# Kernel optimization log

Measured on AMD Instinct MI355X. Metric: run time of the kernel, lower is better.

The kernel has to match this reference:

```python
import jax, jax.numpy as jnp
import numpy as np

B, T, C, H = 8, 2048, 1024, 128


def setup_inputs() -> dict:
    key = jax.random.key(0)
    k1, k2, k3, k4 = jax.random.split(key, 4)
    x = jax.random.normal(k1, (B, T, C), dtype=jnp.float32)
    # torch nn.Linear(n_embed, head_size, bias=False) weights, stored as [C, H] for x @ W
    scale = 1.0 / np.sqrt(C)
    Wk = jax.random.normal(k2, (C, H), dtype=jnp.float32) * scale
    Wq = jax.random.normal(k3, (C, H), dtype=jnp.float32) * scale
    Wv = jax.random.normal(k4, (C, H), dtype=jnp.float32) * scale
    return {"x": x, "Wk": Wk, "Wq": Wq, "Wv": Wv}


def reference(x, Wk, Wq, Wv):
    # Faithful translation of Head.forward (dropout = identity in eval mode).
    Bx, Tx, Cx = x.shape
    k = x @ Wk  # [B,T,H]
    q = x @ Wq  # [B,T,H]
    v = x @ Wv  # [B,T,H]
    # NOTE: original scales by C**-0.5 (n_embed), not head_size**-0.5.
    scores = jnp.einsum('bth,bsh->bts', q, k) * (Cx ** -0.5)  # [B,T,T]
    causal = jnp.tril(jnp.ones((Tx, Tx), dtype=bool))  # tril buffer
    scores = jnp.where(causal, scores, -jnp.inf)
    weights = jax.nn.softmax(scores, axis=-1)
    out = jnp.einsum('bts,bsh->bth', weights, v)  # [B,T,H]
    return out
```

## Files before the change

### kernel.cpp

```cpp
#include <hip/hip_runtime.h>
#include <type_traits>

#define Bn 8
#define Tn 2048
#define Cn 1024
#define Hn 128
#define Mn (Bn*Tn)

typedef __attribute__((ext_vector_type(4))) float f32x4;
typedef __attribute__((ext_vector_type(2))) float f32x2;
typedef __attribute__((ext_vector_type(16))) float f32x16;
typedef __attribute__((ext_vector_type(8))) short s16x8;
typedef __attribute__((ext_vector_type(4))) int i32x4;
typedef __attribute__((ext_vector_type(2))) int i32x2;
typedef unsigned int u32;

__device__ __forceinline__ unsigned short f2bf(float f) {
  union { float f; unsigned u; } v; v.f = f;
  unsigned r = v.u + 0x7FFFu + ((v.u >> 16) & 1u);
  return (unsigned short)(r >> 16);
}

__device__ __forceinline__ unsigned cvtpk(float lo, float hi) {
  unsigned r;
  asm("v_cvt_pk_bf16_f32 %0, %1, %2" : "=v"(r) : "v"(lo), "v"(hi));
  return r;
}

__device__ __forceinline__ i32x2 swap32(int a, int b) {
#if __has_builtin(__builtin_amdgcn_permlane32_swap)
  return __builtin_amdgcn_permlane32_swap(a, b, false, false);
#else
  int ax = __shfl_xor(a, 32), bx = __shfl_xor(b, 32);
  i32x2 r;
  r[0] = (threadIdx.x & 32) ? bx : a;
  r[1] = (threadIdx.x & 32) ? b : ax;
  return r;
#endif
}

__device__ __forceinline__ void gl_lds16(const void* g, void* l) {
  __builtin_amdgcn_global_load_lds((const __attribute__((address_space(1))) u32*)g,
                                   (__attribute__((address_space(3))) u32*)l, 16, 0, 0);
}

__global__ __launch_bounds__(256) void prep_wt(const float* __restrict__ Wq,
                                               const float* __restrict__ Wk,
                                               const float* __restrict__ Wv,
                                               unsigned short* __restrict__ Wt) {
  __shared__ float tile[64][33];
  const int w = blockIdx.z;
  const float* W = (w == 0) ? Wq : (w == 1) ? Wk : Wv;
  const float scale = (w == 0) ? 0.03125f : 1.0f;
  const int c0 = blockIdx.x * 64, h0 = blockIdx.y * 32;
  const int tid = threadIdx.x;
  const int hl = tid & 31, cg = tid >> 5;
#pragma unroll
  for (int i = 0; i < 8; i++) {
    int cl = cg * 8 + i;
    tile[cl][hl] = W[(c0 + cl) * Hn + h0 + hl];
  }
  __syncthreads();
  const int cl2 = tid & 63, hg = tid >> 6;
#pragma unroll
  for (int i = 0; i < 8; i++) {
    int hl2 = hg * 8 + i;
    Wt[(size_t)(w * Hn + h0 + hl2) * Cn + c0 + cl2] = f2bf(tile[cl2][hl2] * scale);
  }
}

__global__ __launch_bounds__(256, 2) void proj_fused(const float* __restrict__ x,
                                                     const unsigned short* __restrict__ Wt,
                                                     unsigned short* __restrict__ qkv) {
  __shared__ __align__(16) unsigned short Abuf[2][64 * 64];
  __shared__ __align__(16) unsigned short Bbuf[2][192 * 64];
  const int tid = threadIdx.x;
  const int lane = tid & 63, wv = tid >> 6;
  const int wm = wv >> 1, wn = wv & 1;
  const int l31 = lane & 31, hi = lane >> 5;
  const int bm = blockIdx.x * 64;
  const int bn = blockIdx.y * 192;

  f32x16 acc[3];
#pragma unroll
  for (int i = 0; i < 3; i++)
#pragma unroll
    for (int r = 0; r < 16; r++) acc[i][r] = 0.f;

  auto stageB = [&](int buf, int kk) {
#pragma unroll
    for (int i = 0; i < 6; i++) {
      int r0 = wv * 48 + i * 8;
      int row = r0 + (lane >> 3);
      const unsigned short* src = Wt + (size_t)(bn + row) * Cn + kk + (((lane & 7) ^ (row & 7)) << 3);
      gl_lds16(src, &Bbuf[buf][r0 * 64]);
    }
  };
  auto loadA = [&](int kk, float4& v0, float4& v1, float4& v2, float4& v3) {
    int r0 = tid >> 3, s0 = tid & 7;
    const float* g0 = x + (size_t)(bm + r0) * Cn + kk + s0 * 8;
    int r1 = r0 + 32;
    const float* g1 = x + (size_t)(bm + r1) * Cn + kk + s0 * 8;
    v0 = *(const float4*)g0;
    v1 = *(const float4*)(g0 + 4);
    v2 = *(const float4*)g1;
    v3 = *(const float4*)(g1 + 4);
  };
  auto writeA = [&](int buf, float4 v0, float4 v1, float4 v2, float4 v3) {
    int r0 = tid >> 3, s0 = tid & 7;
    int r1 = r0 + 32;
    i32x4 w0 = {(int)cvtpk(v0.x, v0.y), (int)cvtpk(v0.z, v0.w),
                (int)cvtpk(v1.x, v1.y), (int)cvtpk(v1.z, v1.w)};
    i32x4 w1 = {(int)cvtpk(v2.x, v2.y), (int)cvtpk(v2.z, v2.w),
                (int)cvtpk(v3.x, v3.y), (int)cvtpk(v3.z, v3.w)};
    *(i32x4*)&Abuf[buf][r0 * 64 + ((s0 ^ (r0 & 7)) << 3)] = w0;
    *(i32x4*)&Abuf[buf][r1 * 64 + ((s0 ^ (r1 & 7)) << 3)] = w1;
  };

  {
    float4 a0, a1, a2, a3;
    loadA(0, a0, a1, a2, a3);
    stageB(0, 0);
    writeA(0, a0, a1, a2, a3);
  }
  __syncthreads();

#pragma unroll 2
  for (int t = 0; t < 16; t++) {
    const int cur = t & 1, nxt = cur ^ 1;
    const bool more = (t < 15);
    float4 a0, a1, a2, a3;
    if (more) {
      loadA((t + 1) * 64, a0, a1, a2, a3);
      stageB(nxt, (t + 1) * 64);
    }
    const unsigned short* Ab = Abuf[cur];
    const unsigned short* Bb = Bbuf[cur];
    s16x8 aF[4];
    const int arow = wm * 32 + l31;
#pragma unroll
    for (int ks = 0; ks < 4; ks++)
      aF[ks] = *(const s16x8*)&Ab[arow * 64 + (((ks * 2 + hi) ^ (arow & 7)) << 3)];
    __builtin_amdgcn_s_setprio(1);
#pragma unroll
    for (int ks = 0; ks < 4; ks++)
#pragma unroll
      for (int ni = 0; ni < 3; ni++) {
        int brow = wn * 96 + ni * 32 + l31;
        s16x8 bF = *(const s16x8*)&Bb[brow * 64 + (((ks * 2 + hi) ^ (brow & 7)) << 3)];
        acc[ni] = __builtin_amdgcn_mfma_f32_32x32x16_bf16(aF[ks], bF, acc[ni], 0, 0, 0);
      }
    __builtin_amdgcn_s_setprio(0);
    if (more) {
      writeA(nxt, a0, a1, a2, a3);
      __syncthreads();
    }
  }

#pragma unroll
  for (int ni = 0; ni < 3; ni++) {
    const int cb = blockIdx.y * 6 + wn * 3 + ni;
    if (cb < 8) {
      const int w = cb >> 2;
      const int h = (cb & 3) * 32 + l31;
      unsigned short* o = qkv + (size_t)w * ((size_t)Mn * Hn);
#pragma unroll
      for (int r = 0; r < 16; r++) {
        int m = bm + wm * 32 + (r & 3) + 8 * (r >> 2) + 4 * hi;
        o[(size_t)m * Hn + h] = f2bf(acc[ni][r]);
      }
    } else {
      const int h = (cb - 8) * 32 + l31;
      const int bb = bm >> 11;
      const int tl0 = (bm & 2047) + wm * 32;
      unsigned short* vt = qkv + (size_t)2 * Mn * Hn + (size_t)bb * (Hn * Tn) + (size_t)h * Tn;
#pragma unroll
      for (int r = 0; r < 16; r++)
        vt[tl0 + (r & 3) + 8 * (r >> 2) + 4 * hi] = f2bf(acc[ni][r]);
    }
  }
}

__global__ __launch_bounds__(256, 2) void attn_fwd(const unsigned short* __restrict__ qkv,
                                                   float* __restrict__ o_part,
                                                   float* __restrict__ ml,
                                                   int sshift) {
  __shared__ __align__(16) unsigned short Kl[2][64 * 128];
  __shared__ __align__(16) unsigned short Vl[2][128 * 64];

  const int bid = blockIdx.x;
  const int b = bid & 7;
  const int r = bid >> 3;
  const int jj = r & 15;
  const int sp = r >> 4;
  const int S = 1 << sshift;
  const int j = (S > 1 && sp >= (S >> 1)) ? (15 - jj) : jj;
  const int s = sp;

  const int tid = threadIdx.x;
  const int lane = tid & 63, wv = tid >> 6;
  const int l31 = lane & 31, hi = lane >> 5;

  const unsigned short* qb  = qkv + (size_t)b * (Tn * Hn);
  const unsigned short* kb  = qkv + (size_t)(Mn * Hn) + (size_t)b * (Tn * Hn);
  const unsigned short* vtb = qkv + (size_t)2 * (Mn * Hn) + (size_t)b * (Hn * Tn);

  const int qrow0 = j * 128 + wv * 32;
  const int qg = qrow0 + l31;

  const int ntt = (j + 1) * 2;
  const int tlo = (s * ntt) >> sshift;
  const int thi = ((s + 1) * ntt) >> sshift;

  f32x16 oT[4];
#pragma unroll
  for (int i = 0; i < 4; i++)
#pragma unroll
    for (int q = 0; q < 16; q++) oT[i][q] = 0.f;
  float m_ = -1e30f, l_ = 0.f;

  auto stage = [&](int buf, int tile) {
    const int kvb0 = tile * 64;
#pragma unroll
    for (int i = 0; i < 4; i++) {
      int r0 = wv * 16 + i * 4;
      int row = r0 + (lane >> 4);
      int ch = lane & 15;
      const unsigned short* src = kb + (size_t)(kvb0 + row) * Hn + ((ch ^ (row & 7)) << 3);
      gl_lds16(src, &Kl[buf][r0 * 128]);
    }
#pragma unroll
    for (int i = 0; i < 4; i++) {
      int r0 = wv * 32 + i * 8;
      int row = r0 + (lane >> 3);
      int ch = lane & 7;
      const unsigned short* src = vtb + (size_t)row * Tn + kvb0 + ((ch ^ (row & 7)) << 3);
      gl_lds16(src, &Vl[buf][r0 * 64]);
    }
  };

  if (tlo < thi) {
    s16x8 qB[8];
#pragma unroll
    for (int hs = 0; hs < 8; hs++)
      qB[hs] = *(const s16x8*)(qb + (size_t)qg * Hn + hs * 16 + hi * 8);

    stage(0, tlo);
    asm volatile("s_waitcnt vmcnt(0)");
    __syncthreads();
    int buf = 0;

    for (int t = tlo; t < thi; t++) {
      if (t + 1 < thi) stage(buf ^ 1, t + 1);
      const int kvb = t * 64;
      if (kvb < qrow0 + 32) {
        const unsigned short* Kb = &Kl[buf][0];
        f32x16 sv0, sv1;
#pragma unroll
        for (int q = 0; q < 16; q++) { sv0[q] = 0.f; sv1[q] = 0.f; }
        __builtin_amdgcn_s_setprio(1);
        {
          const int row = l31;
#pragma unroll
          for (int hs = 0; hs < 8; hs++) {
            s16x8 kf = *(const s16x8*)&Kb[row * 128 + (((hs * 2 + hi) ^ (row & 7)) << 3)];
            sv0 = __builtin_amdgcn_mfma_f32_32x32x16_bf16(kf, qB[hs], sv0, 0, 0, 0);
          }
        }
        {
          const int row = 32 + l31;
#pragma unroll
          for (int hs = 0; hs < 8; hs++) {
            s16x8 kf = *(const s16x8*)&Kb[row * 128 + (((hs * 2 + hi) ^ (row & 7)) << 3)];
            sv1 = __builtin_amdgcn_mfma_f32_32x32x16_bf16(kf, qB[hs], sv1, 0, 0, 0);
          }
        }
        __builtin_amdgcn_s_setprio(0);
        if (kvb + 63 > qrow0) {
#pragma unroll
          for (int q = 0; q < 16; q++) {
            int kr = (q & 3) + 8 * (q >> 2) + 4 * hi;
            if (kvb + kr > qg) sv0[q] = -1e30f;
            if (kvb + 32 + kr > qg) sv1[q] = -1e30f;
          }
        }
        float om = sv0[0];
#pragma unroll
        for (int q = 1; q < 16; q++) om = fmaxf(om, sv0[q]);
#pragma unroll
        for (int q = 0; q < 16; q++) om = fmaxf(om, sv1[q]);
        i32x2 mx = swap32(__builtin_bit_cast(int, om), __builtin_bit_cast(int, om));
        float pm = __builtin_bit_cast(float, hi ? mx[0] : mx[1]);
        float tmax = fmaxf(om, pm);
        if (__any(tmax > m_ + 8.f)) {
          float mn = fmaxf(m_, tmax);
          float sc = __expf(m_ - mn);
          m_ = mn; l_ *= sc;
#pragma unroll
          for (int i = 0; i < 4; i++)
#pragma unroll
            for (int q = 0; q < 16; q++) oT[i][q] *= sc;
        }
        float osum = 0.f;
#pragma unroll
        for (int q = 0; q < 16; q++) { sv0[q] = __expf(sv0[q] - m_); osum += sv0[q]; }
#pragma unroll
        for (int q = 0; q < 16; q++) { sv1[q] = __expf(sv1[q] - m_); osum += sv1[q]; }
        i32x2 sx = swap32(__builtin_bit_cast(int, osum), __builtin_bit_cast(int, osum));
        float psum = __builtin_bit_cast(float, hi ? sx[0] : sx[1]);
        l_ += osum + psum;
        s16x8 pB[4];
        {
          unsigned PK[8];
#pragma unroll
          for (int n = 0; n < 8; n++) PK[n] = cvtpk(sv0[2 * n], sv0[2 * n + 1]);
          i32x2 e0 = swap32((int)PK[0], (int)PK[2]);
          i32x2 e1 = swap32((int)PK[1], (int)PK[3]);
          i32x2 e2 = swap32((int)PK[4], (int)PK[6]);
          i32x2 e3 = swap32((int)PK[5], (int)PK[7]);
          i32x4 w0 = {e0[0], e1[0], e0[1], e1[1]};
          i32x4 w1 = {e2[0], e3[0], e2[1], e3[1]};
          pB[0] = __builtin_bit_cast(s16x8, w0);
          pB[1] = __builtin_bit_cast(s16x8, w1);
        }
        {
          unsigned PK[8];
#pragma unroll
          for (int n = 0; n < 8; n++) PK[n] = cvtpk(sv1[2 * n], sv1[2 * n + 1]);
          i32x2 e0 = swap32((int)PK[0], (int)PK[2]);
          i32x2 e1 = swap32((int)PK[1], (int)PK[3]);
          i32x2 e2 = swap32((int)PK[4], (int)PK[6]);
          i32x2 e3 = swap32((int)PK[5], (int)PK[7]);
          i32x4 w0 = {e0[0], e1[0], e0[1], e1[1]};
          i32x4 w1 = {e2[0], e3[0], e2[1], e3[1]};
          pB[2] = __builtin_bit_cast(s16x8, w0);
          pB[3] = __builtin_bit_cast(s16x8, w1);
        }
        __builtin_amdgcn_s_setprio(1);
#pragma unroll
        for (int hsl = 0; hsl < 4; hsl++) {
          const int row = hsl * 32 + l31;
#pragma unroll
          for (int ks = 0; ks < 4; ks++) {
            s16x8 vf = *(const s16x8*)&Vl[buf][row * 64 + (((ks * 2 + hi) ^ (row & 7)) << 3)];
            oT[hsl] = __builtin_amdgcn_mfma_f32_32x32x16_bf16(vf, pB[ks], oT[hsl], 0, 0, 0);
          }
        }
        __builtin_amdgcn_s_setprio(0);
      }
      asm volatile("s_waitcnt vmcnt(0)");
      __syncthreads();
      buf ^= 1;
    }
  }

  float* orow = o_part + (size_t)s * ((size_t)Mn * Hn) + (size_t)(b * Tn + qg) * Hn;
#pragma unroll
  for (int hsl = 0; hsl < 4; hsl++)
#pragma unroll
    for (int g = 0; g < 4; g++) {
      f32x4 st = {oT[hsl][4 * g + 0], oT[hsl][4 * g + 1], oT[hsl][4 * g + 2], oT[hsl][4 * g + 3]};
      *(f32x4*)(orow + hsl * 32 + g * 8 + hi * 4) = st;
    }
  if (lane < 32) {
    f32x2 w = {m_, l_};
    *(f32x2*)(ml + (size_t)s * (Mn * 2) + (size_t)(b * Tn + qg) * 2) = w;
  }
}

__global__ __launch_bounds__(256) void combine(const float* __restrict__ o_part,
                                               const float* __restrict__ ml,
                                               float* __restrict__ out, int S) {
  const int q = blockIdx.x * 2 + (threadIdx.x >> 7);
  const int h = threadIdx.x & 127;
  float M = -1e30f;
  for (int s = 0; s < S; s++) M = fmaxf(M, ml[(size_t)s * (Mn * 2) + q * 2]);
  float L = 0.f, acc = 0.f;
  for (int s = 0; s < S; s++) {
    float ms = ml[(size_t)s * (Mn * 2) + q * 2];
    float ls = ml[(size_t)s * (Mn * 2) + q * 2 + 1];
    float w = __expf(ms - M);
    L += ls * w;
    acc += o_part[(size_t)s * ((size_t)Mn * Hn) + (size_t)q * Hn + h] * w;
  }
  out[(size_t)q * Hn + h] = acc / L;
}

extern "C" void kernel_launch(void* const* d_in, const int* in_sizes, int n_in,
                              void* d_out, int out_size, void* d_ws, size_t ws_size,
                              hipStream_t stream) {
  const float* x  = (const float*)d_in[0];
  const float* Wk = (const float*)d_in[1];
  const float* Wq = (const float*)d_in[2];
  const float* Wv = (const float*)d_in[3];
  float* out = (float*)d_out;

  char* ws = (char*)d_ws;
  const size_t wt_b  = 786432;
  const size_t qkv_b = (size_t)3 * Mn * Hn * 2;
  const size_t base  = wt_b + qkv_b;
  const size_t per   = (size_t)Mn * Hn * 4 + (size_t)Mn * 8;
  int sshift = (ws_size >= base + 4 * per) ? 2 : (ws_size >= base + 2 * per) ? 1 : 0;
  const int S = 1 << sshift;

  unsigned short* Wt  = (unsigned short*)ws;
  unsigned short* qkv = (unsigned short*)(ws + wt_b);
  float* o_part = (float*)(ws + base);
  float* mlp    = (float*)(ws + base + (size_t)S * Mn * Hn * 4);

  prep_wt<<<dim3(16, 4, 3), 256, 0, stream>>>(Wq, Wk, Wv, Wt);
  proj_fused<<<dim3(256, 2), 256, 0, stream>>>(x, Wt, qkv);
  attn_fwd<<<128 * S, 256, 0, stream>>>(qkv, o_part, mlp, sshift);
  combine<<<Mn / 2, 256, 0, stream>>>(o_part, mlp, out, S);
}
```

Measured before the change: 73.51 us.

## Load projection weight fragments directly from global, remap blocks across XCDs

The projection kernel stops staging the weight tile in LDS and reads B fragments for each MFMA straight from global memory through per-wave pointers. The A tile from x is now prefetched two steps ahead using two register sets. The grid becomes 1D with an XCD-aware mapping, so the two N-halves of the same M strip run on the same XCD and can share L2. This frees LDS and removes the async copies, but it makes the MFMA loop depend on global load latency and uses more registers.

```diff
diff --git a/kernel.cpp b/kernel.cpp
--- a/kernel.cpp
+++ b/kernel.cpp
@@ -73,13 +73,21 @@
                                                      const unsigned short* __restrict__ Wt,
                                                      unsigned short* __restrict__ qkv) {
   __shared__ __align__(16) unsigned short Abuf[2][64 * 64];
-  __shared__ __align__(16) unsigned short Bbuf[2][192 * 64];
   const int tid = threadIdx.x;
   const int lane = tid & 63, wv = tid >> 6;
   const int wm = wv >> 1, wn = wv & 1;
   const int l31 = lane & 31, hi = lane >> 5;
-  const int bm = blockIdx.x * 64;
-  const int bn = blockIdx.y * 192;
+
+  const int bid = blockIdx.x;
+  const int xcd = bid & 7, idx = bid >> 3;
+  const int mstr = xcd + 8 * (idx >> 1);
+  const int ny = idx & 1;
+  const int bm = mstr * 64;
+  const int bn = ny * 192;
+
+  const unsigned short* bptr0 = Wt + (size_t)(bn + wn * 96 + 0 * 32 + l31) * Cn + hi * 8;
+  const unsigned short* bptr1 = Wt + (size_t)(bn + wn * 96 + 1 * 32 + l31) * Cn + hi * 8;
+  const unsigned short* bptr2 = Wt + (size_t)(bn + wn * 96 + 2 * 32 + l31) * Cn + hi * 8;
 
   f32x16 acc[3];
 #pragma unroll
@@ -87,79 +95,69 @@
 #pragma unroll
     for (int r = 0; r < 16; r++) acc[i][r] = 0.f;
 
-  auto stageB = [&](int buf, int kk) {
-#pragma unroll
-    for (int i = 0; i < 6; i++) {
-      int r0 = wv * 48 + i * 8;
-      int row = r0 + (lane >> 3);
-      const unsigned short* src = Wt + (size_t)(bn + row) * Cn + kk + (((lane & 7) ^ (row & 7)) << 3);
-      gl_lds16(src, &Bbuf[buf][r0 * 64]);
-    }
+  const int ar0 = tid >> 3, as0 = tid & 7;
+
+  auto loadA = [&](int t, float4* R) {
+    const int kk = (t <= 15 ? t : 15) * 64;
+    const float* g0 = x + (size_t)(bm + ar0) * Cn + kk + as0 * 8;
+    const float* g1 = x + (size_t)(bm + ar0 + 32) * Cn + kk + as0 * 8;
+    R[0] = *(const float4*)g0;
+    R[1] = *(const float4*)(g0 + 4);
+    R[2] = *(const float4*)g1;
+    R[3] = *(const float4*)(g1 + 4);
   };
-  auto loadA = [&](int kk, float4& v0, float4& v1, float4& v2, float4& v3) {
-    int r0 = tid >> 3, s0 = tid & 7;
-    const float* g0 = x + (size_t)(bm + r0) * Cn + kk + s0 * 8;
-    int r1 = r0 + 32;
-    const float* g1 = x + (size_t)(bm + r1) * Cn + kk + s0 * 8;
-    v0 = *(const float4*)g0;
-    v1 = *(const float4*)(g0 + 4);
-    v2 = *(const float4*)g1;
-    v3 = *(const float4*)(g1 + 4);
+  auto writeA = [&](int buf, const float4* R) {
+    i32x4 w0 = {(int)cvtpk(R[0].x, R[0].y), (int)cvtpk(R[0].z, R[0].w),
+                (int)cvtpk(R[1].x, R[1].y), (int)cvtpk(R[1].z, R[1].w)};
+    i32x4 w1 = {(int)cvtpk(R[2].x, R[2].y), (int)cvtpk(R[2].z, R[2].w),
+                (int)cvtpk(R[3].x, R[3].y), (int)cvtpk(R[3].z, R[3].w)};
+    *(i32x4*)&Abuf[buf][ar0 * 64 + ((as0 ^ (ar0 & 7)) << 3)] = w0;
+    *(i32x4*)&Abuf[buf][(ar0 + 32) * 64 + ((as0 ^ ((ar0 + 32) & 7)) << 3)] = w1;
   };
-  auto writeA = [&](int buf, float4 v0, float4 v1, float4 v2, float4 v3) {
-    int r0 = tid >> 3, s0 = tid & 7;
-    int r1 = r0 + 32;
-    i32x4 w0 = {(int)cvtpk(v0.x, v0.y), (int)cvtpk(v0.z, v0.w),
-                (int)cvtpk(v1.x, v1.y), (int)cvtpk(v1.z, v1.w)};
-    i32x4 w1 = {(int)cvtpk(v2.x, v2.y), (int)cvtpk(v2.z, v2.w),
-                (int)cvtpk(v3.x, v3.y), (int)cvtpk(v3.z, v3.w)};
-    *(i32x4*)&Abuf[buf][r0 * 64 + ((s0 ^ (r0 & 7)) << 3)] = w0;
-    *(i32x4*)&Abuf[buf][r1 * 64 + ((s0 ^ (r1 & 7)) << 3)] = w1;
-  };
-
-  {
-    float4 a0, a1, a2, a3;
-    loadA(0, a0, a1, a2, a3);
-    stageB(0, 0);
-    writeA(0, a0, a1, a2, a3);
-  }
+
+  float4 RA[4], RB[4];
+  loadA(0, RA);
+  loadA(1, RB);
+  writeA(0, RA);
   __syncthreads();
 
-#pragma unroll 2
-  for (int t = 0; t < 16; t++) {
-    const int cur = t & 1, nxt = cur ^ 1;
+  const int arow = wm * 32 + l31;
+
+  auto body = [&](int t, auto PC) {
+    constexpr int P = decltype(PC)::value;
     const bool more = (t < 15);
-    float4 a0, a1, a2, a3;
-    if (more) {
-      loadA((t + 1) * 64, a0, a1, a2, a3);
-      stageB(nxt, (t + 1) * 64);
-    }
-    const unsigned short* Ab = Abuf[cur];
-    const unsigned short* Bb = Bbuf[cur];
+    if constexpr (P == 0) loadA(t + 2, RA); else loadA(t + 2, RB);
     s16x8 aF[4];
-    const int arow = wm * 32 + l31;
 #pragma unroll
     for (int ks = 0; ks < 4; ks++)
-      aF[ks] = *(const s16x8*)&Ab[arow * 64 + (((ks * 2 + hi) ^ (arow & 7)) << 3)];
+      aF[ks] = *(const s16x8*)&Abuf[P][arow * 64 + (((ks * 2 + hi) ^ (arow & 7)) << 3)];
+    const size_t co = (size_t)t * 64;
     __builtin_amdgcn_s_setprio(1);
 #pragma unroll
-    for (int ks = 0; ks < 4; ks++)
-#pragma unroll
-      for (int ni = 0; ni < 3; ni++) {
-        int brow = wn * 96 + ni * 32 + l31;
-        s16x8 bF = *(const s16x8*)&Bb[brow * 64 + (((ks * 2 + hi) ^ (brow & 7)) << 3)];
-        acc[ni] = __builtin_amdgcn_mfma_f32_32x32x16_bf16(aF[ks], bF, acc[ni], 0, 0, 0);
-      }
+    for (int ks = 0; ks < 4; ks++) {
+      s16x8 b0 = *(const s16x8*)(bptr0 + co + ks * 16);
+      s16x8 b1 = *(const s16x8*)(bptr1 + co + ks * 16);
+      s16x8 b2 = *(const s16x8*)(bptr2 + co + ks * 16);
+      acc[0] = __builtin_amdgcn_mfma_f32_32x32x16_bf16(aF[ks], b0, acc[0], 0, 0, 0);
+      acc[1] = __builtin_amdgcn_mfma_f32_32x32x16_bf16(aF[ks], b1, acc[1], 0, 0, 0);
+      acc[2] = __builtin_amdgcn_mfma_f32_32x32x16_bf16(aF[ks], b2, acc[2], 0, 0, 0);
+    }
     __builtin_amdgcn_s_setprio(0);
     if (more) {
-      writeA(nxt, a0, a1, a2, a3);
+      if constexpr (P == 0) writeA(P ^ 1, RB); else writeA(P ^ 1, RA);
       __syncthreads();
     }
+  };
+
+#pragma unroll 2
+  for (int t = 0; t < 16; t += 2) {
+    body(t, std::integral_constant<int, 0>{});
+    body(t + 1, std::integral_constant<int, 1>{});
   }
 
 #pragma unroll
   for (int ni = 0; ni < 3; ni++) {
-    const int cb = blockIdx.y * 6 + wn * 3 + ni;
+    const int cb = ny * 6 + wn * 3 + ni;
     if (cb < 8) {
       const int w = cb >> 2;
       const int h = (cb & 3) * 32 + l31;
@@ -409,7 +407,7 @@
   float* mlp    = (float*)(ws + base + (size_t)S * Mn * Hn * 4);
 
   prep_wt<<<dim3(16, 4, 3), 256, 0, stream>>>(Wq, Wk, Wv, Wt);
-  proj_fused<<<dim3(256, 2), 256, 0, stream>>>(x, Wt, qkv);
+  proj_fused<<<512, 256, 0, stream>>>(x, Wt, qkv);
   attn_fwd<<<128 * S, 256, 0, stream>>>(qkv, o_part, mlp, sshift);
   combine<<<Mn / 2, 256, 0, stream>>>(o_part, mlp, out, S);
 }
```

Measured after the change: 103.1 us. +40.3%, slower.
